# Optimization experiments

Hardware: AMD Instinct MI355X
Metric: run time of the kernel (lower is better)

## Reference

```python
import jax, jax.numpy as jnp
import numpy as np

B, S, D = 4, 2048, 1024
H = 4 * D          # expert hidden dim
E_SPEC = 4         # num specific experts
E_SHR = 2          # num shared experts
TOP_K = 2


def setup_inputs() -> dict:
    key = jax.random.key(0)
    ks = jax.random.split(key, 16)
    s = 0.02
    return {
        "x": jax.random.normal(ks[0], (B, S, D), jnp.float32),
        # specific experts (stacked over expert axis)
        "spec_w1": jax.random.normal(ks[1], (E_SPEC, D, H), jnp.float32) * s,
        "spec_b1": jnp.zeros((E_SPEC, H), jnp.float32),
        "spec_w2": jax.random.normal(ks[2], (E_SPEC, H, D), jnp.float32) * s,
        "spec_b2": jnp.zeros((E_SPEC, D), jnp.float32),
        "spec_rw": jax.random.normal(ks[3], (D, E_SPEC), jnp.float32) * s,
        "spec_rb": jnp.zeros((E_SPEC,), jnp.float32),
        # shared experts
        "shr_w1": jax.random.normal(ks[4], (E_SHR, D, H), jnp.float32) * s,
        "shr_b1": jnp.zeros((E_SHR, H), jnp.float32),
        "shr_w2": jax.random.normal(ks[5], (E_SHR, H, D), jnp.float32) * s,
        "shr_b2": jnp.zeros((E_SHR, D), jnp.float32),
        "shr_rw": jax.random.normal(ks[6], (D, E_SHR), jnp.float32) * s,
        "shr_rb": jnp.zeros((E_SHR,), jnp.float32),
    }


def _expert_mlp(xf, w1, b1, w2, b2):
    # xf: [T, D]; w1: [E, D, H]; w2: [E, H, D] -> [E, T, D]
    h = jax.nn.gelu(jnp.einsum("td,edh->eth", xf, w1) + b1[:, None, :],
                    approximate=False)
    return jnp.einsum("eth,ehd->etd", h, w2) + b2[:, None, :]


def reference(x, spec_w1, spec_b1, spec_w2, spec_b2, spec_rw, spec_rb,
              shr_w1, shr_b1, shr_w2, shr_b2, shr_rw, shr_rb):
    b, s, d = x.shape
    xf = x.reshape(-1, d)                      # [T, D]
    T = xf.shape[0]

    # --- specific (top-k) routing ---
    spec_probs = jax.nn.softmax(xf @ spec_rw + spec_rb, axis=-1)   # [T, E]
    topk_probs, topk_idx = jax.lax.top_k(spec_probs, TOP_K)        # [T, K]

    # aux load-balancing loss
    counts = jnp.zeros((E_SPEC,), jnp.float32).at[topk_idx.reshape(-1)].add(1.0)
    fraction = counts / (T * TOP_K)
    aux_loss = E_SPEC * jnp.sum(fraction * spec_probs.mean(axis=0))

    # gate[t, e] = sum_k topk_probs[t,k] * 1[topk_idx[t,k]==e]
    gate = jnp.sum(jax.nn.one_hot(topk_idx, E_SPEC, dtype=xf.dtype)
                   * topk_probs[..., None], axis=1)                # [T, E]

    spec_out_e = _expert_mlp(xf, spec_w1, spec_b1, spec_w2, spec_b2)  # [E, T, D]
    specific_out = jnp.einsum("te,etd->td", gate, spec_out_e)

    # --- shared (dense) experts ---
    shr_probs = jax.nn.softmax(xf @ shr_rw + shr_rb, axis=-1)      # [T, E_shr]
    shr_out_e = _expert_mlp(xf, shr_w1, shr_b1, shr_w2, shr_b2)    # [E_shr, T, D]
    shared_out = jnp.einsum("te,etd->td", shr_probs, shr_out_e)

    final = (specific_out + shared_out).reshape(b, s, d)
    return final, aux_loss
```

## Files before the change

### kernel.cpp

```cpp
#include <hip/hip_runtime.h>
#include <hip/hip_bf16.h>

#define T_TOK 8192
#define DDIM 1024
#define HDIM 4096

typedef __bf16 bf16;
typedef bf16 bf16x8 __attribute__((ext_vector_type(8)));
typedef float f32x4 __attribute__((ext_vector_type(4)));

#define ASM_VMCNT(n) asm volatile("s_waitcnt vmcnt(" #n ")" ::: "memory")
#define MFMA16(a, b, c) __builtin_amdgcn_mfma_f32_16x16x32_bf16((a), (b), (c), 0, 0, 0)

__device__ __forceinline__ void gl_lds16(const void* g, void* l) {
  __builtin_amdgcn_global_load_lds(
      (const __attribute__((address_space(1))) unsigned int*)g,
      (__attribute__((address_space(3))) unsigned int*)l, 16, 0, 0);
}

__global__ __launch_bounds__(256) void convert_x(const float* __restrict__ x,
                                                 bf16* __restrict__ xb) {
  const size_t i = ((size_t)blockIdx.x * 256 + threadIdx.x) * 8;
  const float4 v0 = *(const float4*)(x + i);
  const float4 v1 = *(const float4*)(x + i + 4);
  bf16x8 o;
  o[0] = (bf16)v0.x; o[1] = (bf16)v0.y; o[2] = (bf16)v0.z; o[3] = (bf16)v0.w;
  o[4] = (bf16)v1.x; o[5] = (bf16)v1.y; o[6] = (bf16)v1.z; o[7] = (bf16)v1.w;
  *(bf16x8*)(xb + i) = o;
}

__global__ __launch_bounds__(256) void transpose_convert(
    const float* __restrict__ src, bf16* __restrict__ dst, int R, int C) {
  __shared__ float tile[32][33];
  const size_t mat = (size_t)blockIdx.z * R * C;
  const int c0 = blockIdx.x * 32, r0 = blockIdx.y * 32;
  const int tx = threadIdx.x & 31, ty = threadIdx.x >> 5;
#pragma unroll
  for (int i = 0; i < 4; ++i)
    tile[ty + 8 * i][tx] =
        src[mat + (size_t)(r0 + ty + 8 * i) * C + c0 + tx];
  __syncthreads();
#pragma unroll
  for (int i = 0; i < 4; ++i)
    dst[mat + (size_t)(c0 + ty + 8 * i) * R + r0 + tx] =
        (bf16)tile[tx][ty + 8 * i];
}

__global__ __launch_bounds__(256) void router_probs(
    const float* __restrict__ x, const float* __restrict__ srw,
    const float* __restrict__ srb, const float* __restrict__ hrw,
    const float* __restrict__ hrb, float* __restrict__ gate,
    float4* __restrict__ probs4, int* __restrict__ top2) {
  const int lane = threadIdx.x & 63;
  const int w = threadIdx.x >> 6;
  const int t = blockIdx.x * 4 + w;

  const float* xr = x + (size_t)t * DDIM;
  float p0 = 0, p1 = 0, p2 = 0, p3 = 0, p4 = 0, p5 = 0;
#pragma unroll
  for (int c = 0; c < 4; ++c) {
    const int d = c * 256 + lane * 4;
    const float4 xv = *(const float4*)(xr + d);
    const float xa[4] = {xv.x, xv.y, xv.z, xv.w};
#pragma unroll
    for (int j = 0; j < 4; ++j) {
      const float xd = xa[j];
      const float4 r4 = *(const float4*)(srw + (size_t)(d + j) * 4);
      p0 += xd * r4.x; p1 += xd * r4.y; p2 += xd * r4.z; p3 += xd * r4.w;
      const float2 r2 = *(const float2*)(hrw + (size_t)(d + j) * 2);
      p4 += xd * r2.x; p5 += xd * r2.y;
    }
  }
#pragma unroll
  for (int off = 32; off >= 1; off >>= 1) {
    p0 += __shfl_xor(p0, off);
    p1 += __shfl_xor(p1, off);
    p2 += __shfl_xor(p2, off);
    p3 += __shfl_xor(p3, off);
    p4 += __shfl_xor(p4, off);
    p5 += __shfl_xor(p5, off);
  }
  if (lane == 0) {
    const float l0 = p0 + srb[0], l1 = p1 + srb[1];
    const float l2 = p2 + srb[2], l3 = p3 + srb[3];
    const float m = fmaxf(fmaxf(l0, l1), fmaxf(l2, l3));
    const float e0 = expf(l0 - m), e1 = expf(l1 - m);
    const float e2 = expf(l2 - m), e3 = expf(l3 - m);
    const float s = e0 + e1 + e2 + e3;
    float pr[4] = {e0 / s, e1 / s, e2 / s, e3 / s};
    int i1 = 0; float v1 = pr[0];
#pragma unroll
    for (int e = 1; e < 4; ++e) if (pr[e] > v1) { v1 = pr[e]; i1 = e; }
    int i2 = -1; float v2 = -1.0f;
#pragma unroll
    for (int e = 0; e < 4; ++e)
      if (e != i1 && pr[e] > v2) { v2 = pr[e]; i2 = e; }
    float g[4] = {0, 0, 0, 0};
    g[i1] = v1; g[i2] = v2;
    float* gr = gate + (size_t)t * 8;
    gr[0] = g[0]; gr[1] = g[1]; gr[2] = g[2]; gr[3] = g[3];
    const float h0 = p4 + hrb[0], h1 = p5 + hrb[1];
    const float mh = fmaxf(h0, h1);
    const float q0 = expf(h0 - mh), q1 = expf(h1 - mh);
    const float qs = q0 + q1;
    gr[4] = q0 / qs; gr[5] = q1 / qs; gr[6] = 0; gr[7] = 0;
    probs4[t] = make_float4(pr[0], pr[1], pr[2], pr[3]);
    top2[t] = i1 | (i2 << 8);
  }
}

__global__ __launch_bounds__(1024) void scan_build(
    const int* __restrict__ top2, const float4* __restrict__ probs4,
    int* __restrict__ cnt, int* __restrict__ lists, float* __restrict__ auxg) {
  __shared__ unsigned long long sc[1024];
  __shared__ float4 rp[512];
  const int tid = threadIdx.x;

  int ee[8];
  unsigned long long c = 0;
  float4 ps = make_float4(0.f, 0.f, 0.f, 0.f);
#pragma unroll
  for (int j = 0; j < 8; ++j) {
    const int t = tid * 8 + j;
    const int p = top2[t];
    ee[j] = p;
    const int a = p & 15, b = (p >> 8) & 15;
    c += (1ULL << (16 * a)) + (1ULL << (16 * b));
    const float4 pv = probs4[t];
    ps.x += pv.x; ps.y += pv.y; ps.z += pv.z; ps.w += pv.w;
  }
  sc[tid] = c;
  __syncthreads();
  for (int off = 1; off < 1024; off <<= 1) {
    const unsigned long long mine = sc[tid];
    const unsigned long long prev = (tid >= off) ? sc[tid - off] : 0ULL;
    __syncthreads();
    sc[tid] = mine + prev;
    __syncthreads();
  }
  const unsigned long long incl = sc[tid];
  const unsigned long long tot = sc[1023];
  const unsigned long long excl = incl - c;
  int q0 = (int)(excl & 0xffff), q1 = (int)((excl >> 16) & 0xffff);
  int q2 = (int)((excl >> 32) & 0xffff), q3 = (int)((excl >> 48) & 0xffff);
#pragma unroll
  for (int j = 0; j < 8; ++j) {
    const int t = tid * 8 + j;
    const int a = ee[j] & 15, b = (ee[j] >> 8) & 15;
    const int pa = (a == 0) ? q0 : (a == 1) ? q1 : (a == 2) ? q2 : q3;
    lists[a * 8192 + pa] = t;
    q0 += (a == 0); q1 += (a == 1); q2 += (a == 2); q3 += (a == 3);
    const int pb = (b == 0) ? q0 : (b == 1) ? q1 : (b == 2) ? q2 : q3;
    lists[b * 8192 + pb] = t;
    q0 += (b == 0); q1 += (b == 1); q2 += (b == 2); q3 += (b == 3);
  }
  if (tid == 1023) {
    const int c0 = (int)(tot & 0xffff), c1 = (int)((tot >> 16) & 0xffff);
    const int c2 = (int)((tot >> 32) & 0xffff), c3 = (int)((tot >> 48) & 0xffff);
    cnt[0] = c0; cnt[1] = c1; cnt[2] = c2; cnt[3] = c3;
    auxg[0] = (float)c0; auxg[1] = (float)c1;
    auxg[2] = (float)c2; auxg[3] = (float)c3;
  }
  if (tid >= 512) rp[tid - 512] = ps;
  __syncthreads();
  if (tid < 512) {
    const float4 o = rp[tid];
    ps.x += o.x; ps.y += o.y; ps.z += o.z; ps.w += o.w;
  }
  for (int w = 256; w >= 1; w >>= 1) {
    __syncthreads();
    if (tid >= w && tid < 2 * w) rp[tid - w] = ps;
    __syncthreads();
    if (tid < w) {
      const float4 o = rp[tid];
      ps.x += o.x; ps.y += o.y; ps.z += o.z; ps.w += o.w;
    }
  }
  if (tid == 0) {
    auxg[4] = ps.x; auxg[5] = ps.y; auxg[6] = ps.z; auxg[7] = ps.w;
  }
}

__global__ void aux_finalize(const float* __restrict__ auxg,
                             float* __restrict__ outp) {
  float a = 0.0f;
#pragma unroll
  for (int e = 0; e < 4; ++e)
    a += (auxg[e] / (float)(T_TOK * 2)) * (auxg[4 + e] / (float)T_TOK);
  outp[0] = 4.0f * a;
}

template <int BN_, int MODE>
__global__ __launch_bounds__(512, 2) void gemm4p(
    const bf16* __restrict__ A, const bf16* __restrict__ B, int M, int N,
    int K, const float* __restrict__ bias, bf16* __restrict__ Hout,
    float* __restrict__ Fout, const float* __restrict__ gate, int gidx,
    int NBn, int CH_M, int CH_N, const int* __restrict__ cnt,
    const int* __restrict__ lists, int eid) {
  constexpr int NREP = BN_ / 64;
  constexpr int NHF = NREP / 2;
  constexpr int WNT = BN_ / 4;
  constexpr int ABYTES = 256 * 64 * 2;
  constexpr int BBYTES = BN_ * 64 * 2;
  constexpr bool DYN = (MODE == 3 || MODE == 4);

  __shared__ __align__(1024) bf16 Alds[2 * 256 * 64];
  __shared__ __align__(1024) bf16 Blds[2 * BN_ * 64];

  const int tid = threadIdx.x;
  const int lane = tid & 63, wid = tid >> 6;
  const int wm = wid >> 2, wn = wid & 3;
  const int lr = lane & 15, lg = lane >> 4;

  int bm, bn;
  if constexpr (DYN) {
    const int nbm = ((cnt[eid] + 255) & ~255) >> 8;
    const int CHm = (nbm + 3) >> 2;
    constexpr int CHn = (BN_ == 256) ? 8 : 4;
    const int need = 8 * CHm * CHn;
    if (blockIdx.x >= need) return;
    const int xc = blockIdx.x & 7;
    const int idx = blockIdx.x >> 3;
    const int cm = xc >> 1, cn = xc & 1;
    bm = cm * CHm + idx / CHn;
    bn = cn * CHn + idx % CHn;
    if (bm >= nbm) return;
  } else {
    const int xcd = blockIdx.x & 7;
    const int idx = blockIdx.x >> 3;
    const int ncn = NBn / CH_N;
    const int cm = xcd / ncn, cn = xcd % ncn;
    bm = cm * CH_M + idx / CH_N;
    bn = cn * CH_N + idx % CH_N;
  }

  const int NT = K >> 6;

  const int L = tid * 16;
  const int rl = L >> 7;
  const int colb = (L & 127) ^ ((rl & 7) << 4);

  int ar0 = bm * 256 + rl, ar1 = ar0 + 64, ar2 = ar0 + 128, ar3 = ar0 + 192;
  if constexpr (MODE == 4) {
    const int* lp = lists + eid * 8192;
    int t;
    t = lp[ar0]; ar0 = t < 0 ? 0 : t;
    t = lp[ar1]; ar1 = t < 0 ? 0 : t;
    t = lp[ar2]; ar2 = t < 0 ? 0 : t;
    t = lp[ar3]; ar3 = t < 0 ? 0 : t;
  }
  const bf16* sAc0 = A + (size_t)ar0 * K + (colb >> 1);
  const bf16* sAc1 = A + (size_t)ar1 * K + (colb >> 1);
  const bf16* sAc2 = A + (size_t)ar2 * K + (colb >> 1);
  const bf16* sAc3 = A + (size_t)ar3 * K + (colb >> 1);
  const bf16* sB = B + (size_t)(bn * BN_ + rl) * K + (colb >> 1);

  char* const ldsA = (char*)Alds;
  char* const ldsB = (char*)Blds;
  const int wb = wid * 1024;
  char* const stA[2] = {ldsA + wb, ldsA + ABYTES + wb};
  char* const stB[2] = {ldsB + wb, ldsB + BBYTES + wb};

  const int ax0 = (lg * 16) ^ ((lr & 7) << 4);
  const int ax1 = ax0 ^ 64;
  const int aro = (wm * 128 + lr) * 128;
  const int bro = (wn * WNT + lr) * 128;
  const char* const Ak0[2] = {ldsA + aro + ax0, ldsA + ABYTES + aro + ax0};
  const char* const Ak1[2] = {ldsA + aro + ax1, ldsA + ABYTES + aro + ax1};
  const char* const Bk0[2] = {ldsB + bro + ax0, ldsB + BBYTES + bro + ax0};
  const char* const Bk1[2] = {ldsB + bro + ax1, ldsB + BBYTES + bro + ax1};

  f32x4 acc[8][NREP] = {};

  gl_lds16(sAc0, stA[0]);
  gl_lds16(sAc1, stA[0] + 8192);
  gl_lds16(sAc2, stA[0] + 16384);
  gl_lds16(sAc3, stA[0] + 24576);
  gl_lds16(sB, stB[0]);
  gl_lds16(sB + (size_t)64 * K, stB[0] + 8192);
  if constexpr (BN_ == 256) {
    gl_lds16(sB + (size_t)128 * K, stB[0] + 16384);
    gl_lds16(sB + (size_t)192 * K, stB[0] + 24576);
  }
  gl_lds16(sB + 64, stB[1]);
  gl_lds16(sB + (size_t)64 * K + 64, stB[1] + 8192);
  if constexpr (BN_ == 256) {
    gl_lds16(sB + (size_t)128 * K + 64, stB[1] + 16384);
    gl_lds16(sB + (size_t)192 * K + 64, stB[1] + 24576);
  }
  gl_lds16(sAc0 + 64, stA[1]);
  gl_lds16(sAc1 + 64, stA[1] + 8192);
  if constexpr (BN_ == 256) ASM_VMCNT(6); else ASM_VMCNT(4);
  __builtin_amdgcn_s_barrier();

  for (int kt0 = 0; kt0 < NT; kt0 += 2) {
#pragma unroll
    for (int par = 0; par < 2; ++par) {
      const int kt = kt0 + par;
      const int cur = par, oth = par ^ 1;
      const bool st1 = (kt + 1) < NT, st2 = (kt + 2) < NT;
      const size_t ko1 = (size_t)(kt + 1) << 6, ko2 = (size_t)(kt + 2) << 6;
      const char* Ac0 = Ak0[cur]; const char* Ac1 = Ak1[cur];
      const char* Bc0 = Bk0[cur]; const char* Bc1 = Bk1[cur];

      bf16x8 af[4][2], bfr[NREP][2];

#pragma unroll
      for (int mf = 0; mf < 4; ++mf) {
        af[mf][0] = *(const bf16x8*)(Ac0 + mf * 2048);
        af[mf][1] = *(const bf16x8*)(Ac1 + mf * 2048);
      }
#pragma unroll
      for (int nf = 0; nf < NHF; ++nf) {
        bfr[nf][0] = *(const bf16x8*)(Bc0 + nf * 2048);
        bfr[nf][1] = *(const bf16x8*)(Bc1 + nf * 2048);
      }
      if (st1) {
        gl_lds16(sAc2 + ko1, stA[oth] + 16384);
        gl_lds16(sAc3 + ko1, stA[oth] + 24576);
      }
      __builtin_amdgcn_s_barrier();
      asm volatile("s_waitcnt lgkmcnt(0)" ::: "memory");
      __builtin_amdgcn_sched_barrier(0);
      __builtin_amdgcn_s_setprio(1);
#pragma unroll
      for (int mf = 0; mf < 4; ++mf)
#pragma unroll
        for (int nf = 0; nf < NHF; ++nf) {
          acc[mf][nf] = MFMA16(af[mf][0], bfr[nf][0], acc[mf][nf]);
          acc[mf][nf] = MFMA16(af[mf][1], bfr[nf][1], acc[mf][nf]);
        }
      __builtin_amdgcn_s_setprio(0);
      __builtin_amdgcn_s_barrier();

#pragma unroll
      for (int nf = NHF; nf < NREP; ++nf) {
        bfr[nf][0] = *(const bf16x8*)(Bc0 + nf * 2048);
        bfr[nf][1] = *(const bf16x8*)(Bc1 + nf * 2048);
      }
      __builtin_amdgcn_s_barrier();
      asm volatile("s_waitcnt lgkmcnt(0)" ::: "memory");
      __builtin_amdgcn_sched_barrier(0);
      __builtin_amdgcn_s_setprio(1);
#pragma unroll
      for (int mf = 0; mf < 4; ++mf)
#pragma unroll
        for (int nf = NHF; nf < NREP; ++nf) {
          acc[mf][nf] = MFMA16(af[mf][0], bfr[nf][0], acc[mf][nf]);
          acc[mf][nf] = MFMA16(af[mf][1], bfr[nf][1], acc[mf][nf]);
        }
      __builtin_amdgcn_s_setprio(0);
      __builtin_amdgcn_s_barrier();

#pragma unroll
      for (int mf = 0; mf < 4; ++mf) {
        af[mf][0] = *(const bf16x8*)(Ac0 + 8192 + mf * 2048);
        af[mf][1] = *(const bf16x8*)(Ac1 + 8192 + mf * 2048);
      }
      if (st2) {
        gl_lds16(sB + ko2, stB[cur]);
        gl_lds16(sB + (size_t)64 * K + ko2, stB[cur] + 8192);
      }
      __builtin_amdgcn_s_barrier();
      asm volatile("s_waitcnt lgkmcnt(0)" ::: "memory");
      __builtin_amdgcn_sched_barrier(0);
      __builtin_amdgcn_s_setprio(1);
#pragma unroll
      for (int mf = 0; mf < 4; ++mf)
#pragma unroll
        for (int nf = 0; nf < NHF; ++nf) {
          acc[4 + mf][nf] = MFMA16(af[mf][0], bfr[nf][0], acc[4 + mf][nf]);
          acc[4 + mf][nf] = MFMA16(af[mf][1], bfr[nf][1], acc[4 + mf][nf]);
        }
      __builtin_amdgcn_s_setprio(0);
      __builtin_amdgcn_s_barrier();

      if (st2) {
        if constexpr (BN_ == 256) {
          gl_lds16(sB + (size_t)128 * K + ko2, stB[cur] + 16384);
          gl_lds16(sB + (size_t)192 * K + ko2, stB[cur] + 24576);
        }
        gl_lds16(sAc0 + ko2, stA[cur]);
        gl_lds16(sAc1 + ko2, stA[cur] + 8192);
      }
      __builtin_amdgcn_s_setprio(1);
#pragma unroll
      for (int mf = 0; mf < 4; ++mf)
#pragma unroll
        for (int nf = NHF; nf < NREP; ++nf) {
          acc[4 + mf][nf] = MFMA16(af[mf][0], bfr[nf][0], acc[4 + mf][nf]);
          acc[4 + mf][nf] = MFMA16(af[mf][1], bfr[nf][1], acc[4 + mf][nf]);
        }
      __builtin_amdgcn_s_setprio(0);
      if (st2) {
        if constexpr (BN_ == 256) ASM_VMCNT(6); else ASM_VMCNT(4);
        __builtin_amdgcn_s_barrier();
      } else if (st1) {
        ASM_VMCNT(0);
        __builtin_amdgcn_s_barrier();
      }
    }
  }

  const int colb2 = bn * BN_ + wn * WNT;
  const int rowb = bm * 256 + wm * 128 + lg * 4;
  float bv[NREP];
#pragma unroll
  for (int nf = 0; nf < NREP; ++nf) bv[nf] = bias[colb2 + nf * 16 + lr];
#pragma unroll
  for (int mf = 0; mf < 8; ++mf) {
    if constexpr (MODE == 0 || MODE == 4) {
#pragma unroll
      for (int nf = 0; nf < NREP; ++nf) {
        const int col = colb2 + nf * 16 + lr;
#pragma unroll
        for (int r = 0; r < 4; ++r) {
          const int row = rowb + mf * 16 + r;
          const float v = acc[mf][nf][r] + bv[nf];
          const float gl = 0.5f * v * (1.0f + erff(v * 0.7071067811865475f));
          Hout[(size_t)row * N + col] = (bf16)gl;
        }
      }
    } else if constexpr (MODE == 1 || MODE == 2) {
      float gv[4];
#pragma unroll
      for (int r = 0; r < 4; ++r)
        gv[r] = gate[(size_t)(rowb + mf * 16 + r) * 8 + gidx];
#pragma unroll
      for (int nf = 0; nf < NREP; ++nf) {
        const int col = colb2 + nf * 16 + lr;
#pragma unroll
        for (int r = 0; r < 4; ++r) {
          const float v = acc[mf][nf][r] + bv[nf];
          const size_t oi = (size_t)(rowb + mf * 16 + r) * N + col;
          if constexpr (MODE == 1)
            Fout[oi] += gv[r] * v;
          else
            Fout[oi] = gv[r] * v;
        }
      }
    } else {
      const int* lp = lists + eid * 8192;
      int tok[4]; float gv[4];
#pragma unroll
      for (int r = 0; r < 4; ++r) {
        tok[r] = lp[rowb + mf * 16 + r];
        gv[r] = tok[r] >= 0 ? gate[(size_t)tok[r] * 8 + gidx] : 0.0f;
      }
#pragma unroll
      for (int nf = 0; nf < NREP; ++nf) {
        const int col = colb2 + nf * 16 + lr;
#pragma unroll
        for (int r = 0; r < 4; ++r) {
          if (tok[r] >= 0) {
            const float v = acc[mf][nf][r] + bv[nf];
            Fout[(size_t)tok[r] * N + col] += gv[r] * v;
          }
        }
      }
    }
  }
}

extern "C" void kernel_launch(void* const* d_in, const int* in_sizes, int n_in,
                              void* d_out, int out_size, void* d_ws,
                              size_t ws_size, hipStream_t stream) {
  const float* x = (const float*)d_in[0];
  const float* spec_w1 = (const float*)d_in[1];
  const float* spec_b1 = (const float*)d_in[2];
  const float* spec_w2 = (const float*)d_in[3];
  const float* spec_b2 = (const float*)d_in[4];
  const float* spec_rw = (const float*)d_in[5];
  const float* spec_rb = (const float*)d_in[6];
  const float* shr_w1 = (const float*)d_in[7];
  const float* shr_b1 = (const float*)d_in[8];
  const float* shr_w2 = (const float*)d_in[9];
  const float* shr_b2 = (const float*)d_in[10];
  const float* shr_rw = (const float*)d_in[11];
  const float* shr_rb = (const float*)d_in[12];
  float* out = (float*)d_out;

  char* ws = (char*)d_ws;
  const size_t OFF_W1 = 16777216;
  const size_t OFF_W2 = OFF_W1 + 50331648;
  const size_t OFF_H = OFF_W2 + 50331648;
  const size_t OFF_GATE = OFF_H + 67108864;
  const size_t OFF_AUX = OFF_GATE + 262144;
  const size_t OFF_CNT = OFF_AUX + 64;
  const size_t OFF_LIST = OFF_CNT + 64;
  const size_t OFF_T2 = OFF_LIST + 131072;
  const size_t OFF_P4 = OFF_T2 + 32768;
  bf16* xb = (bf16*)ws;
  bf16* w1t = (bf16*)(ws + OFF_W1);
  bf16* w2t = (bf16*)(ws + OFF_W2);
  bf16* hbuf = (bf16*)(ws + OFF_H);
  float* gate = (float*)(ws + OFF_GATE);
  float* auxg = (float*)(ws + OFF_AUX);
  int* cnt = (int*)(ws + OFF_CNT);
  int* lists = (int*)(ws + OFF_LIST);
  int* top2 = (int*)(ws + OFF_T2);
  float4* probs4 = (float4*)(ws + OFF_P4);

  hipMemsetAsync(lists, 0xFF, 4 * 8192 * 4, stream);

  convert_x<<<(T_TOK * DDIM) / 2048, 256, 0, stream>>>(x, xb);
  transpose_convert<<<dim3(HDIM / 32, DDIM / 32, 4), 256, 0, stream>>>(
      spec_w1, w1t, DDIM, HDIM);
  transpose_convert<<<dim3(HDIM / 32, DDIM / 32, 2), 256, 0, stream>>>(
      shr_w1, w1t + (size_t)4 * DDIM * HDIM, DDIM, HDIM);
  transpose_convert<<<dim3(DDIM / 32, HDIM / 32, 4), 256, 0, stream>>>(
      spec_w2, w2t, HDIM, DDIM);
  transpose_convert<<<dim3(DDIM / 32, HDIM / 32, 2), 256, 0, stream>>>(
      shr_w2, w2t + (size_t)4 * DDIM * HDIM, HDIM, DDIM);

  router_probs<<<T_TOK / 4, 256, 0, stream>>>(x, spec_rw, spec_rb, shr_rw,
                                              shr_rb, gate, probs4, top2);
  scan_build<<<1, 1024, 0, stream>>>(top2, probs4, cnt, lists, auxg);

  for (int es = 0; es < 2; ++es) {
    const bf16* w1e = w1t + (size_t)(4 + es) * DDIM * HDIM;
    const bf16* w2e = w2t + (size_t)(4 + es) * DDIM * HDIM;
    const float* b1e = shr_b1 + (size_t)es * HDIM;
    const float* b2e = shr_b2 + (size_t)es * DDIM;
    gemm4p<256, 0><<<512, 512, 0, stream>>>(
        xb, w1e, T_TOK, HDIM, DDIM, b1e, hbuf, nullptr, nullptr, 0,
        16, 8, 8, nullptr, nullptr, 0);
    if (es == 0)
      gemm4p<128, 2><<<256, 512, 0, stream>>>(
          hbuf, w2e, T_TOK, DDIM, HDIM, b2e, nullptr, out, gate, 4,
          8, 8, 4, nullptr, nullptr, 0);
    else
      gemm4p<128, 1><<<256, 512, 0, stream>>>(
          hbuf, w2e, T_TOK, DDIM, HDIM, b2e, nullptr, out, gate, 5,
          8, 8, 4, nullptr, nullptr, 0);
  }

  for (int e = 0; e < 4; ++e) {
    const bf16* w1e = w1t + (size_t)e * DDIM * HDIM;
    const bf16* w2e = w2t + (size_t)e * DDIM * HDIM;
    const float* b1e = spec_b1 + (size_t)e * HDIM;
    const float* b2e = spec_b2 + (size_t)e * DDIM;
    gemm4p<256, 4><<<512, 512, 0, stream>>>(
        xb, w1e, T_TOK, HDIM, DDIM, b1e, hbuf, nullptr, nullptr, 0,
        16, 0, 0, cnt, lists, e);
    gemm4p<128, 3><<<256, 512, 0, stream>>>(
        hbuf, w2e, T_TOK, DDIM, HDIM, b2e, nullptr, out, gate, e,
        8, 0, 0, cnt, lists, e);
  }
  aux_finalize<<<1, 1, 0, stream>>>(auxg, out + (size_t)T_TOK * DDIM);
}
```

Baseline: 1.106 ms.

## Replace first-layer expert GEMM with smaller-tile single-buffered kernel

Adds a new gemmv kernel with 128x128 tiles, K-step 32, 256 threads and no double buffering, and uses it for the first (GELU) GEMM of both the shared and the specific experts in place of the 256x256 double-buffered gemm4p. The GELU epilogue and the gathered-row mode move into the new kernel, and gemm4p loses those modes. The smaller tiles give more blocks and higher occupancy, and the gathered expert rows are padded to multiples of 128 instead of 256, so less padded work is done. In exchange, each tile reuses its data less, and the kernel loses load/compute overlap because it issues two barriers per K-step with no prefetch.

After: 1.059 ms. -4.2%, faster.

```diff
diff --git a/kernel.cpp b/kernel.cpp
--- a/kernel.cpp
+++ b/kernel.cpp
@@ -190,6 +190,104 @@
   outp[0] = 4.0f * a;
 }
 
+template <int MODE>
+__global__ __launch_bounds__(256, 3) void gemmv(
+    const bf16* __restrict__ A, const bf16* __restrict__ B, int N, int K,
+    const float* __restrict__ bias, bf16* __restrict__ Hout, int NBn,
+    int CH_M, int CH_N, const int* __restrict__ cnt,
+    const int* __restrict__ lists, int eid) {
+  __shared__ __align__(1024) bf16 As[128 * 32];
+  __shared__ __align__(1024) bf16 Bs[128 * 32];
+
+  const int tid = threadIdx.x;
+  const int lane = tid & 63, wid = tid >> 6;
+  const int wm = wid >> 1, wn = wid & 1;
+  const int lr = lane & 15, lg = lane >> 4;
+
+  int bm, bn;
+  if constexpr (MODE == 4) {
+    const int nbm = ((cnt[eid] + 127) & ~127) >> 7;
+    const int CHm = (nbm + 3) >> 2;
+    const int need = 8 * CHm * CH_N;
+    if (blockIdx.x >= need) return;
+    const int xc = blockIdx.x & 7;
+    const int idx = blockIdx.x >> 3;
+    bm = (xc >> 1) * CHm + idx / CH_N;
+    bn = (xc & 1) * CH_N + idx % CH_N;
+    if (bm >= nbm) return;
+  } else {
+    const int xcd = blockIdx.x & 7;
+    const int idx = blockIdx.x >> 3;
+    const int ncn = NBn / CH_N;
+    bm = (xcd / ncn) * CH_M + idx / CH_N;
+    bn = (xcd % ncn) * CH_N + idx % CH_N;
+  }
+
+  const int rl = tid >> 2;
+  const int c = ((tid & 3) * 16) ^ (((rl >> 1) & 3) << 4);
+  int ar0 = bm * 128 + rl, ar1 = ar0 + 64;
+  if constexpr (MODE == 4) {
+    const int* lp = lists + eid * 8192;
+    int t = lp[ar0]; ar0 = t < 0 ? 0 : t;
+    t = lp[ar1]; ar1 = t < 0 ? 0 : t;
+  }
+  const bf16* sA0 = A + (size_t)ar0 * K + (c >> 1);
+  const bf16* sA1 = A + (size_t)ar1 * K + (c >> 1);
+  const bf16* sB0 = B + (size_t)(bn * 128 + rl) * K + (c >> 1);
+  const bf16* sB1 = B + (size_t)(bn * 128 + 64 + rl) * K + (c >> 1);
+  char* const dA0 = (char*)As + wid * 1024;
+  char* const dA1 = (char*)As + 4096 + wid * 1024;
+  char* const dB0 = (char*)Bs + wid * 1024;
+  char* const dB1 = (char*)Bs + 4096 + wid * 1024;
+
+  const int rkey = ((lr >> 1) & 3) << 4;
+  const char* Ard = (const char*)As + (wm * 64 + lr) * 64 + ((lg * 16) ^ rkey);
+  const char* Brd = (const char*)Bs + (wn * 64 + lr) * 64 + ((lg * 16) ^ rkey);
+
+  f32x4 acc[4][4] = {};
+  const int NT = K >> 5;
+  for (int kt = 0; kt < NT; ++kt) {
+    const int ko = kt << 5;
+    gl_lds16(sA0 + ko, dA0);
+    gl_lds16(sA1 + ko, dA1);
+    gl_lds16(sB0 + ko, dB0);
+    gl_lds16(sB1 + ko, dB1);
+    __syncthreads();
+    bf16x8 af[4], bfr[4];
+#pragma unroll
+    for (int mf = 0; mf < 4; ++mf) af[mf] = *(const bf16x8*)(Ard + mf * 1024);
+#pragma unroll
+    for (int nf = 0; nf < 4; ++nf) bfr[nf] = *(const bf16x8*)(Brd + nf * 1024);
+    __builtin_amdgcn_s_setprio(1);
+#pragma unroll
+    for (int mf = 0; mf < 4; ++mf)
+#pragma unroll
+      for (int nf = 0; nf < 4; ++nf)
+        acc[mf][nf] = MFMA16(af[mf], bfr[nf], acc[mf][nf]);
+    __builtin_amdgcn_s_setprio(0);
+    __syncthreads();
+  }
+
+  const int colb = bn * 128 + wn * 64;
+  const int rowb = bm * 128 + wm * 64 + lg * 4;
+  float bv[4];
+#pragma unroll
+  for (int nf = 0; nf < 4; ++nf) bv[nf] = bias[colb + nf * 16 + lr];
+#pragma unroll
+  for (int mf = 0; mf < 4; ++mf)
+#pragma unroll
+    for (int nf = 0; nf < 4; ++nf) {
+      const int col = colb + nf * 16 + lr;
+#pragma unroll
+      for (int r = 0; r < 4; ++r) {
+        const int row = rowb + mf * 16 + r;
+        const float v = acc[mf][nf][r] + bv[nf];
+        const float gl = 0.5f * v * (1.0f + erff(v * 0.7071067811865475f));
+        Hout[(size_t)row * N + col] = (bf16)gl;
+      }
+    }
+}
+
 template <int BN_, int MODE>
 __global__ __launch_bounds__(512, 2) void gemm4p(
     const bf16* __restrict__ A, const bf16* __restrict__ B, int M, int N,
@@ -202,7 +300,7 @@
   constexpr int WNT = BN_ / 4;
   constexpr int ABYTES = 256 * 64 * 2;
   constexpr int BBYTES = BN_ * 64 * 2;
-  constexpr bool DYN = (MODE == 3 || MODE == 4);
+  constexpr bool DYN = (MODE == 3);
 
   __shared__ __align__(1024) bf16 Alds[2 * 256 * 64];
   __shared__ __align__(1024) bf16 Blds[2 * BN_ * 64];
@@ -221,17 +319,15 @@
     if (blockIdx.x >= need) return;
     const int xc = blockIdx.x & 7;
     const int idx = blockIdx.x >> 3;
-    const int cm = xc >> 1, cn = xc & 1;
-    bm = cm * CHm + idx / CHn;
-    bn = cn * CHn + idx % CHn;
+    bm = (xc >> 1) * CHm + idx / CHn;
+    bn = (xc & 1) * CHn + idx % CHn;
     if (bm >= nbm) return;
   } else {
     const int xcd = blockIdx.x & 7;
     const int idx = blockIdx.x >> 3;
     const int ncn = NBn / CH_N;
-    const int cm = xcd / ncn, cn = xcd % ncn;
-    bm = cm * CH_M + idx / CH_N;
-    bn = cn * CH_N + idx % CH_N;
+    bm = (xcd / ncn) * CH_M + idx / CH_N;
+    bn = (xcd % ncn) * CH_N + idx % CH_N;
   }
 
   const int NT = K >> 6;
@@ -240,19 +336,11 @@
   const int rl = L >> 7;
   const int colb = (L & 127) ^ ((rl & 7) << 4);
 
-  int ar0 = bm * 256 + rl, ar1 = ar0 + 64, ar2 = ar0 + 128, ar3 = ar0 + 192;
-  if constexpr (MODE == 4) {
-    const int* lp = lists + eid * 8192;
-    int t;
-    t = lp[ar0]; ar0 = t < 0 ? 0 : t;
-    t = lp[ar1]; ar1 = t < 0 ? 0 : t;
-    t = lp[ar2]; ar2 = t < 0 ? 0 : t;
-    t = lp[ar3]; ar3 = t < 0 ? 0 : t;
-  }
+  const int ar0 = bm * 256 + rl;
   const bf16* sAc0 = A + (size_t)ar0 * K + (colb >> 1);
-  const bf16* sAc1 = A + (size_t)ar1 * K + (colb >> 1);
-  const bf16* sAc2 = A + (size_t)ar2 * K + (colb >> 1);
-  const bf16* sAc3 = A + (size_t)ar3 * K + (colb >> 1);
+  const bf16* sAc1 = A + (size_t)(ar0 + 64) * K + (colb >> 1);
+  const bf16* sAc2 = A + (size_t)(ar0 + 128) * K + (colb >> 1);
+  const bf16* sAc3 = A + (size_t)(ar0 + 192) * K + (colb >> 1);
   const bf16* sB = B + (size_t)(bn * BN_ + rl) * K + (colb >> 1);
 
   char* const ldsA = (char*)Alds;
@@ -409,19 +497,7 @@
   for (int nf = 0; nf < NREP; ++nf) bv[nf] = bias[colb2 + nf * 16 + lr];
 #pragma unroll
   for (int mf = 0; mf < 8; ++mf) {
-    if constexpr (MODE == 0 || MODE == 4) {
-#pragma unroll
-      for (int nf = 0; nf < NREP; ++nf) {
-        const int col = colb2 + nf * 16 + lr;
-#pragma unroll
-        for (int r = 0; r < 4; ++r) {
-          const int row = rowb + mf * 16 + r;
-          const float v = acc[mf][nf][r] + bv[nf];
-          const float gl = 0.5f * v * (1.0f + erff(v * 0.7071067811865475f));
-          Hout[(size_t)row * N + col] = (bf16)gl;
-        }
-      }
-    } else if constexpr (MODE == 1 || MODE == 2) {
+    if constexpr (MODE == 1 || MODE == 2) {
       float gv[4];
 #pragma unroll
       for (int r = 0; r < 4; ++r)
@@ -522,9 +598,8 @@
     const bf16* w2e = w2t + (size_t)(4 + es) * DDIM * HDIM;
     const float* b1e = shr_b1 + (size_t)es * HDIM;
     const float* b2e = shr_b2 + (size_t)es * DDIM;
-    gemm4p<256, 0><<<512, 512, 0, stream>>>(
-        xb, w1e, T_TOK, HDIM, DDIM, b1e, hbuf, nullptr, nullptr, 0,
-        16, 8, 8, nullptr, nullptr, 0);
+    gemmv<0><<<2048, 256, 0, stream>>>(xb, w1e, HDIM, DDIM, b1e, hbuf,
+                                       32, 16, 16, nullptr, nullptr, 0);
     if (es == 0)
       gemm4p<128, 2><<<256, 512, 0, stream>>>(
           hbuf, w2e, T_TOK, DDIM, HDIM, b2e, nullptr, out, gate, 4,
@@ -540,9 +615,8 @@
     const bf16* w2e = w2t + (size_t)e * DDIM * HDIM;
     const float* b1e = spec_b1 + (size_t)e * HDIM;
     const float* b2e = spec_b2 + (size_t)e * DDIM;
-    gemm4p<256, 4><<<512, 512, 0, stream>>>(
-        xb, w1e, T_TOK, HDIM, DDIM, b1e, hbuf, nullptr, nullptr, 0,
-        16, 0, 0, cnt, lists, e);
+    gemmv<4><<<2048, 256, 0, stream>>>(xb, w1e, HDIM, DDIM, b1e, hbuf,
+                                       32, 0, 16, cnt, lists, e);
     gemm4p<128, 3><<<256, 512, 0, stream>>>(
         hbuf, w2e, T_TOK, DDIM, HDIM, b2e, nullptr, out, gate, e,
         8, 0, 0, cnt, lists, e);
```
